# Optimization experiments

Hardware: AMD Instinct MI355X
Metric: run time of the kernel (lower is better)

The kernel has to match this reference:

```python
import jax, jax.numpy as jnp
import numpy as np

N_NODES = 100000
N_EDGES = 1600000
F_IN = 64
HIDDEN = 64
N_CLASSES = 2


def setup_inputs() -> dict:
    key = jax.random.key(0)
    k1, k2, k3, k4, k5, k6 = jax.random.split(key, 6)
    x = jax.random.normal(k1, (N_NODES, F_IN), dtype=jnp.float32)
    edge_index = jax.random.randint(k2, (2, N_EDGES), 0, N_NODES, dtype=jnp.int64)
    # Glorot-ish init for GCNConv linear weights, zero bias (PyG default)
    W1 = jax.random.normal(k3, (F_IN, HIDDEN), dtype=jnp.float32) * (1.0 / np.sqrt(F_IN))
    b1 = jnp.zeros((HIDDEN,), dtype=jnp.float32)
    W2 = jax.random.normal(k4, (HIDDEN, N_CLASSES), dtype=jnp.float32) * (1.0 / np.sqrt(HIDDEN))
    b2 = jnp.zeros((N_CLASSES,), dtype=jnp.float32)
    return {"x": x, "edge_index": edge_index, "W1": W1, "b1": b1, "W2": W2, "b2": b2}


def _gcn_norm(edge_index, num_nodes):
    # Add self-loops, then symmetric normalization D^-1/2 (A+I) D^-1/2
    loops = jnp.arange(num_nodes, dtype=edge_index.dtype)
    row = jnp.concatenate([edge_index[0], loops])  # [E+N] targets
    col = jnp.concatenate([edge_index[1], loops])  # [E+N] sources
    deg = jax.ops.segment_sum(jnp.ones(row.shape[0], jnp.float32), row, num_segments=num_nodes)
    dinv = jnp.where(deg > 0, jax.lax.rsqrt(deg), 0.0)
    norm = dinv[row] * dinv[col]  # [E+N]
    return row, col, norm


def _gcn_conv(x, W, b, row, col, norm, num_nodes):
    h = x @ W                                   # [N, out]
    msg = h[col] * norm[:, None]                # gather + scale, [E+N, out]
    agg = jax.ops.segment_sum(msg, row, num_segments=num_nodes)  # scatter-add
    return agg + b


def reference(x, edge_index, W1, b1, W2, b2):
    n = x.shape[0]
    row, col, norm = _gcn_norm(edge_index, n)
    h = jax.nn.relu(_gcn_conv(x, W1, b1, row, col, norm, n))
    # dropout p=0.5 is identity in eval mode
    logits = _gcn_conv(h, W2, b2, row, col, norm, n)
    return jax.nn.softmax(logits, axis=1)
```

## Files before the change

kernel.cpp:

```cpp
#include <hip/hip_runtime.h>
#include <hip/hip_fp16.h>


#define NBKT(n) (((n) + 255) >> 8)

typedef _Float16 f16x8 __attribute__((ext_vector_type(8)));
typedef float f32x4 __attribute__((ext_vector_type(4)));

__global__ __launch_bounds__(256) void k_bucketcount(const int* __restrict__ row,
                                                     int* __restrict__ bcnt,
                                                     __half* __restrict__ hp,
                                                     int E, int nb, int N) {
    __shared__ int cnt[392];
    int tid = threadIdx.x;
    int base = blockIdx.x * 4096;
    int m = E - base; if (m > 4096) m = 4096;
    for (int t = tid; t < nb; t += 256) cnt[t] = 0;
    __syncthreads();
    for (int i = tid; i < m; i += 256) atomicAdd(&cnt[row[base + i] >> 8], 1);
    __syncthreads();
    for (int t = tid; t < nb; t += 256) {
        int v = cnt[t];
        if (v > 0) atomicAdd(&bcnt[t], v);
    }
    if (blockIdx.x == 0 && tid < 32) ((int*)(hp + (size_t)N * 64))[tid] = 0;
}

__global__ __launch_bounds__(256) void k_bin(const int* __restrict__ row,
                                             const int* __restrict__ col,
                                             const int* __restrict__ bcnt,
                                             int* __restrict__ relcur,
                                             unsigned* __restrict__ pairbuf,
                                             int E, int nb) {
    __shared__ unsigned items[4096];
    __shared__ unsigned short bktid[4096];
    __shared__ int cnt[392];
    __shared__ int start0[392];
    __shared__ int cursor[392];
    __shared__ int gb[392];
    __shared__ int gbase[392];

    int tid = threadIdx.x;
    int base = blockIdx.x * 4096;
    int m = E - base; if (m > 4096) m = 4096;

    for (int t = tid; t < nb; t += 256) cnt[t] = 0;
    __syncthreads();
    for (int i = tid; i < m; i += 256) atomicAdd(&cnt[row[base + i] >> 8], 1);
    __syncthreads();
    if (tid < 64) {
        int lane = tid, running = 0;
        for (int ch = 0; ch < 7; ++ch) {
            int idx = ch * 64 + lane;
            int v = (idx < nb) ? cnt[idx] : 0;
            int s = v;
#pragma unroll
            for (int off = 1; off < 64; off <<= 1) {
                int t = __shfl_up(s, off, 64);
                if (lane >= off) s += t;
            }
            if (idx < nb) { start0[idx] = running + s - v; cursor[idx] = running + s - v; }
            running += __shfl(s, 63, 64);
        }
    } else if (tid < 128) {
        int lane = tid - 64, running = 0;
        for (int ch = 0; ch < 7; ++ch) {
            int idx = ch * 64 + lane;
            int v = (idx < nb) ? bcnt[idx] : 0;
            int s = v;
#pragma unroll
            for (int off = 1; off < 64; off <<= 1) {
                int t = __shfl_up(s, off, 64);
                if (lane >= off) s += t;
            }
            if (idx < nb) gb[idx] = running + s - v;
            running += __shfl(s, 63, 64);
        }
    }
    __syncthreads();
    for (int i = tid; i < m; i += 256) {
        int r = row[base + i];
        int c = col[base + i];
        int b = r >> 8;
        int pos = atomicAdd(&cursor[b], 1);
        items[pos] = ((unsigned)(r & 255) << 24) | (unsigned)c;
        bktid[pos] = (unsigned short)b;
    }
    __syncthreads();
    for (int t = tid; t < nb; t += 256) {
        int cv = cnt[t];
        if (cv > 0) gbase[t] = gb[t] + atomicAdd(&relcur[t], cv);
    }
    __syncthreads();
    for (int i = tid; i < m; i += 256) {
        int b = bktid[i];
        pairbuf[gbase[b] + (i - start0[b])] = items[i];
    }
}

__global__ __launch_bounds__(256) void k_sortnode(const unsigned* __restrict__ pairbuf,
                                                  const int* __restrict__ bcnt,
                                                  int* __restrict__ scol,
                                                  int* __restrict__ offsets,
                                                  float* __restrict__ dinv,
                                                  int N, int E) {
    __shared__ int ps[256];
    __shared__ int cnt[256];
    __shared__ int tmp[256];
    __shared__ int cur[256];
    int b = blockIdx.x;
    int tid = threadIdx.x;
    int v = (tid < b) ? bcnt[tid] : 0;
    if (tid + 256 < b) v += bcnt[tid + 256];
    ps[tid] = v;
    __syncthreads();
    for (int s = 128; s >= 1; s >>= 1) {
        if (tid < s) ps[tid] += ps[tid + s];
        __syncthreads();
    }
    int lo = ps[0];
    int hi = lo + bcnt[b];
    cnt[tid] = 0;
    __syncthreads();
    for (int i = lo + tid; i < hi; i += 256)
        atomicAdd(&cnt[pairbuf[i] >> 24], 1);
    __syncthreads();
    int cv = cnt[tid];
    tmp[tid] = cv;
    __syncthreads();
    for (int d = 1; d < 256; d <<= 1) {
        int t = (tid >= (unsigned)d) ? tmp[tid - d] : 0;
        __syncthreads();
        if (tid >= (unsigned)d) tmp[tid] += t;
        __syncthreads();
    }
    int excl = tmp[tid] - cv;
    int n = (b << 8) + tid;
    if (n < N) {
        offsets[n] = lo + excl;
        dinv[n] = rsqrtf((float)(cv + 1));
    }
    cur[tid] = lo + excl;
    if (b == 0 && tid == 0) { offsets[N] = E; scol[E] = N; }
    __syncthreads();
    for (int i = lo + tid; i < hi; i += 256) {
        unsigned it = pairbuf[i];
        int pos = atomicAdd(&cur[it >> 24], 1);
        scol[pos] = (int)(it & 0xFFFFFFu);
    }
}

__global__ __launch_bounds__(256, 2) void k_gemm1(const float* __restrict__ x,
                                                  const float* __restrict__ W1,
                                                  const float* __restrict__ dinv,
                                                  __half* __restrict__ hp, int N) {
    int lane = threadIdx.x & 63;
    int q = lane >> 4;
    int m = lane & 15;
    f16x8 bf[4][2];
#pragma unroll
    for (int nt = 0; nt < 4; ++nt)
#pragma unroll
        for (int kk = 0; kk < 2; ++kk)
#pragma unroll
            for (int j = 0; j < 8; ++j)
                bf[nt][kk][j] = (_Float16)W1[(kk * 32 + q * 8 + j) * 64 + nt * 16 + m];
    int wv = (int)((blockIdx.x * 256 + threadIdx.x) >> 6);
    int nw = (int)((gridDim.x * 256) >> 6);
    int T = N >> 4;
    for (int t = wv; t < T; t += nw) {
        const float* xrow = x + (size_t)(t * 16 + m) * 64;
        float4 u0 = *(const float4*)(xrow + q * 8);
        float4 u1 = *(const float4*)(xrow + q * 8 + 4);
        float4 u2 = *(const float4*)(xrow + 32 + q * 8);
        float4 u3 = *(const float4*)(xrow + 32 + q * 8 + 4);
        f16x8 a0, a1;
        a0[0] = (_Float16)u0.x; a0[1] = (_Float16)u0.y; a0[2] = (_Float16)u0.z; a0[3] = (_Float16)u0.w;
        a0[4] = (_Float16)u1.x; a0[5] = (_Float16)u1.y; a0[6] = (_Float16)u1.z; a0[7] = (_Float16)u1.w;
        a1[0] = (_Float16)u2.x; a1[1] = (_Float16)u2.y; a1[2] = (_Float16)u2.z; a1[3] = (_Float16)u2.w;
        a1[4] = (_Float16)u3.x; a1[5] = (_Float16)u3.y; a1[6] = (_Float16)u3.z; a1[7] = (_Float16)u3.w;
        f32x4 ac0 = {0.f, 0.f, 0.f, 0.f}, ac1 = ac0, ac2 = ac0, ac3 = ac0;
        ac0 = __builtin_amdgcn_mfma_f32_16x16x32_f16(a0, bf[0][0], ac0, 0, 0, 0);
        ac1 = __builtin_amdgcn_mfma_f32_16x16x32_f16(a0, bf[1][0], ac1, 0, 0, 0);
        ac2 = __builtin_amdgcn_mfma_f32_16x16x32_f16(a0, bf[2][0], ac2, 0, 0, 0);
        ac3 = __builtin_amdgcn_mfma_f32_16x16x32_f16(a0, bf[3][0], ac3, 0, 0, 0);
        ac0 = __builtin_amdgcn_mfma_f32_16x16x32_f16(a1, bf[0][1], ac0, 0, 0, 0);
        ac1 = __builtin_amdgcn_mfma_f32_16x16x32_f16(a1, bf[1][1], ac1, 0, 0, 0);
        ac2 = __builtin_amdgcn_mfma_f32_16x16x32_f16(a1, bf[2][1], ac2, 0, 0, 0);
        ac3 = __builtin_amdgcn_mfma_f32_16x16x32_f16(a1, bf[3][1], ac3, 0, 0, 0);
#pragma unroll
        for (int reg = 0; reg < 4; ++reg) {
            int rr = t * 16 + q * 4 + reg;
            float dv = dinv[rr];
            __half* dst = hp + (size_t)rr * 64 + m;
            dst[0]  = __float2half(dv * ac0[reg]);
            dst[16] = __float2half(dv * ac1[reg]);
            dst[32] = __float2half(dv * ac2[reg]);
            dst[48] = __float2half(dv * ac3[reg]);
        }
    }
}

__global__ __launch_bounds__(256) void k_agg1(const __half* __restrict__ hp,
                                              const int* __restrict__ offsets,
                                              const int* __restrict__ sorted_col,
                                              const float* __restrict__ dinv,
                                              const float* __restrict__ b1,
                                              const float* __restrict__ W2,
                                              float2* __restrict__ h2p, int N, int E) {
    int lane = threadIdx.x & 63;
    int slot = lane >> 3;
    int chunk = lane & 7;
    int wid = (int)((blockIdx.x * 256 + threadIdx.x) >> 6);
    int n = wid * 8 + slot;
    int nc = (n < N) ? n : N;
    int start = offsets[nc];
    int end = offsets[(n < N) ? (n + 1) : N];
    int deg = end - start;
    int maxd = deg;
#pragma unroll
    for (int s = 8; s <= 32; s <<= 1) {
        int o = __shfl_xor(maxd, s, 64);
        maxd = (o > maxd) ? o : maxd;
    }
    const float4* hp4 = (const float4*)hp;
    float4 sr = hp4[(size_t)nc * 8 + chunk];
    __half2 acc0 = ((const __half2*)&sr)[0];
    __half2 acc1 = ((const __half2*)&sr)[1];
    __half2 acc2 = ((const __half2*)&sr)[2];
    __half2 acc3 = ((const __half2*)&sr)[3];
    for (int j0 = 0; j0 < maxd; j0 += 4) {
        int a0 = (j0 + 0 < deg) ? (start + j0 + 0) : E;
        int a1 = (j0 + 1 < deg) ? (start + j0 + 1) : E;
        int a2 = (j0 + 2 < deg) ? (start + j0 + 2) : E;
        int a3 = (j0 + 3 < deg) ? (start + j0 + 3) : E;
        int c0 = sorted_col[a0];
        int c1 = sorted_col[a1];
        int c2 = sorted_col[a2];
        int c3 = sorted_col[a3];
        float4 r0 = hp4[(size_t)c0 * 8 + chunk];
        float4 r1 = hp4[(size_t)c1 * 8 + chunk];
        float4 r2 = hp4[(size_t)c2 * 8 + chunk];
        float4 r3 = hp4[(size_t)c3 * 8 + chunk];
        const __half2* h0 = (const __half2*)&r0;
        const __half2* h1_ = (const __half2*)&r1;
        const __half2* h2_ = (const __half2*)&r2;
        const __half2* h3 = (const __half2*)&r3;
        acc0 = __hadd2(acc0, h0[0]); acc1 = __hadd2(acc1, h0[1]);
        acc2 = __hadd2(acc2, h0[2]); acc3 = __hadd2(acc3, h0[3]);
        acc0 = __hadd2(acc0, h1_[0]); acc1 = __hadd2(acc1, h1_[1]);
        acc2 = __hadd2(acc2, h1_[2]); acc3 = __hadd2(acc3, h1_[3]);
        acc0 = __hadd2(acc0, h2_[0]); acc1 = __hadd2(acc1, h2_[1]);
        acc2 = __hadd2(acc2, h2_[2]); acc3 = __hadd2(acc3, h2_[3]);
        acc0 = __hadd2(acc0, h3[0]); acc1 = __hadd2(acc1, h3[1]);
        acc2 = __hadd2(acc2, h3[2]); acc3 = __hadd2(acc3, h3[3]);
    }
    float af[8];
    { float2 f;
      f = __half22float2(acc0); af[0] = f.x; af[1] = f.y;
      f = __half22float2(acc1); af[2] = f.x; af[3] = f.y;
      f = __half22float2(acc2); af[4] = f.x; af[5] = f.y;
      f = __half22float2(acc3); af[6] = f.x; af[7] = f.y; }
    float dn = dinv[(n < N) ? n : (N - 1)];
    float4 b1a = ((const float4*)b1)[chunk * 2];
    float4 b1b = ((const float4*)b1)[chunk * 2 + 1];
    float h1[8];
    h1[0] = fmaxf(fmaf(dn, af[0], b1a.x), 0.f);
    h1[1] = fmaxf(fmaf(dn, af[1], b1a.y), 0.f);
    h1[2] = fmaxf(fmaf(dn, af[2], b1a.z), 0.f);
    h1[3] = fmaxf(fmaf(dn, af[3], b1a.w), 0.f);
    h1[4] = fmaxf(fmaf(dn, af[4], b1b.x), 0.f);
    h1[5] = fmaxf(fmaf(dn, af[5], b1b.y), 0.f);
    h1[6] = fmaxf(fmaf(dn, af[6], b1b.z), 0.f);
    h1[7] = fmaxf(fmaf(dn, af[7], b1b.w), 0.f);
    float p0 = 0.f, p1 = 0.f;
#pragma unroll
    for (int k = 0; k < 4; ++k) {
        float4 w = ((const float4*)W2)[chunk * 4 + k];
        p0 = fmaf(h1[2 * k], w.x, p0); p1 = fmaf(h1[2 * k], w.y, p1);
        p0 = fmaf(h1[2 * k + 1], w.z, p0); p1 = fmaf(h1[2 * k + 1], w.w, p1);
    }
#pragma unroll
    for (int s = 1; s <= 4; s <<= 1) {
        p0 += __shfl_xor(p0, s, 64);
        p1 += __shfl_xor(p1, s, 64);
    }
    if (chunk == 0 && n < N) h2p[n] = make_float2(dn * p0, dn * p1);
}

__global__ __launch_bounds__(256) void k_agg2(const float2* __restrict__ h2p,
                                              const int* __restrict__ offsets,
                                              const int* __restrict__ sorted_col,
                                              const float* __restrict__ dinv,
                                              const float* __restrict__ b2,
                                              float2* __restrict__ out, int N) {
    int gtid = blockIdx.x * 256 + threadIdx.x;
    int n = gtid >> 4;
    int sub = threadIdx.x & 15;
    if (n >= N) return;
    int start = offsets[n], end = offsets[n + 1];
    float ax = 0.f, ay = 0.f;
    if (sub == 0) { float2 s = h2p[n]; ax = s.x; ay = s.y; }
    for (int j = start + sub; j < end; j += 16) {
        float2 v = h2p[sorted_col[j]];
        ax += v.x; ay += v.y;
    }
#pragma unroll
    for (int s = 1; s <= 8; s <<= 1) {
        ax += __shfl_xor(ax, s, 64);
        ay += __shfl_xor(ay, s, 64);
    }
    if (sub == 0) {
        float dn = dinv[n];
        float l0 = fmaf(dn, ax, b2[0]), l1 = fmaf(dn, ay, b2[1]);
        float m = fmaxf(l0, l1);
        float e0 = __expf(l0 - m), e1 = __expf(l1 - m);
        float inv = 1.0f / (e0 + e1);
        out[n] = make_float2(e0 * inv, e1 * inv);
    }
}

extern "C" void kernel_launch(void* const* d_in, const int* in_sizes, int n_in,
                              void* d_out, int out_size, void* d_ws, size_t ws_size,
                              hipStream_t stream) {
    const float* x  = (const float*)d_in[0];
    const int*   ei = (const int*)d_in[1];
    const float* W1 = (const float*)d_in[2];
    const float* b1 = (const float*)d_in[3];
    const float* W2 = (const float*)d_in[4];
    const float* b2 = (const float*)d_in[5];
    float2* out = (float2*)d_out;

    const int N = in_sizes[0] / 64;
    const int E = in_sizes[1] / 2;
    const int nb = NBKT(N);
    const int* row = ei;
    const int* col = ei + E;

    char* p = (char*)d_ws;
    auto alloc = [&](size_t bytes) -> void* {
        void* r = (void*)p;
        p += (bytes + 255) & ~(size_t)255;
        return r;
    };
    int*   bcnt    = (int*)alloc(784 * 4);
    int*   relcur  = bcnt + 392;
    int*   offsets = (int*)alloc((size_t)(N + 1) * 4);
    float* dinv    = (float*)alloc((size_t)N * 4);
    unsigned* pairbuf = (unsigned*)alloc((size_t)E * 4);
    int*   scol    = (int*)alloc((size_t)(E + 1) * 4);
    __half* hp     = (__half*)alloc((size_t)(N + 1) * 64 * 2);
    float2* h2p    = (float2*)alloc((size_t)N * 8);

    const int nTile = (E + 4095) / 4096;

    hipMemsetAsync(bcnt, 0, 784 * 4, stream);
    k_bucketcount<<<nTile, 256, 0, stream>>>(row, bcnt, hp, E, nb, N);
    k_bin<<<nTile, 256, 0, stream>>>(row, col, bcnt, relcur, pairbuf, E, nb);
    k_sortnode<<<nb, 256, 0, stream>>>(pairbuf, bcnt, scol, offsets, dinv, N, E);
    k_gemm1<<<512, 256, 0, stream>>>(x, W1, dinv, hp, N);
    const int nwaves = (N + 7) / 8;
    k_agg1<<<(nwaves + 3) / 4, 256, 0, stream>>>(hp, offsets, scol, dinv, b1, W2, h2p, N, E);
    k_agg2<<<(N * 16 + 255) / 256, 256, 0, stream>>>(h2p, offsets, scol, dinv, b2, out, N);
}
```

Before: 181.8 us.

## Fuse all GCN stages into one persistent kernel with grid-wide barriers

Replaces the six separate kernel launches (bucket count, binning, per-node sort, GEMM1, layer-1 aggregation, layer-2 aggregation) with one persistent kernel of 1120 blocks. The stages are separated by software grid barriers built on global atomics, and shared memory is reused through a union. Binning tiles shrink to 2048 edges, and the GEMM stage appears to stage dinv in LDS. This removes launch gaps and tail effects between short kernels, but relies on every block being co-resident and adds barrier spin cost plus occupancy limits from the fused register and LDS footprint.

```diff
diff --git a/kernel.cpp b/kernel.cpp
--- a/kernel.cpp
+++ b/kernel.cpp
@@ -2,321 +2,332 @@
 #include <hip/hip_fp16.h>
 
 
-#define NBKT(n) (((n) + 255) >> 8)
-
 typedef _Float16 f16x8 __attribute__((ext_vector_type(8)));
 typedef float f32x4 __attribute__((ext_vector_type(4)));
 
-__global__ __launch_bounds__(256) void k_bucketcount(const int* __restrict__ row,
-                                                     int* __restrict__ bcnt,
-                                                     __half* __restrict__ hp,
-                                                     int E, int nb, int N) {
-    __shared__ int cnt[392];
-    int tid = threadIdx.x;
-    int base = blockIdx.x * 4096;
-    int m = E - base; if (m > 4096) m = 4096;
-    for (int t = tid; t < nb; t += 256) cnt[t] = 0;
+#define GRID_BLOCKS 1120
+
+union SmemU {
+    int cnt1[392];
+    struct {
+        unsigned items[2048];
+        unsigned short bktid[2048];
+        int cnt[392];
+        int start0[392];
+        int cursor[392];
+        int gb[392];
+    } p2;
+    struct {
+        int ps[256];
+        int cnt[256];
+        int tmp[256];
+        int cur[256];
+        float sdinv[256];
+    } p3;
+};
+
+__device__ __forceinline__ void gsync(int* bar, int slot) {
     __syncthreads();
-    for (int i = tid; i < m; i += 256) atomicAdd(&cnt[row[base + i] >> 8], 1);
+    if (threadIdx.x == 0) {
+        __threadfence();
+        atomicAdd(&bar[slot], 1);
+        while (atomicAdd(&bar[slot], 0) < (int)gridDim.x)
+            __builtin_amdgcn_s_sleep(2);
+        __threadfence();
+    }
     __syncthreads();
-    for (int t = tid; t < nb; t += 256) {
-        int v = cnt[t];
-        if (v > 0) atomicAdd(&bcnt[t], v);
-    }
-    if (blockIdx.x == 0 && tid < 32) ((int*)(hp + (size_t)N * 64))[tid] = 0;
 }
 
-__global__ __launch_bounds__(256) void k_bin(const int* __restrict__ row,
-                                             const int* __restrict__ col,
-                                             const int* __restrict__ bcnt,
-                                             int* __restrict__ relcur,
-                                             unsigned* __restrict__ pairbuf,
-                                             int E, int nb) {
-    __shared__ unsigned items[4096];
-    __shared__ unsigned short bktid[4096];
-    __shared__ int cnt[392];
-    __shared__ int start0[392];
-    __shared__ int cursor[392];
-    __shared__ int gb[392];
-    __shared__ int gbase[392];
-
-    int tid = threadIdx.x;
-    int base = blockIdx.x * 4096;
-    int m = E - base; if (m > 4096) m = 4096;
-
-    for (int t = tid; t < nb; t += 256) cnt[t] = 0;
-    __syncthreads();
-    for (int i = tid; i < m; i += 256) atomicAdd(&cnt[row[base + i] >> 8], 1);
-    __syncthreads();
-    if (tid < 64) {
-        int lane = tid, running = 0;
-        for (int ch = 0; ch < 7; ++ch) {
-            int idx = ch * 64 + lane;
-            int v = (idx < nb) ? cnt[idx] : 0;
-            int s = v;
-#pragma unroll
-            for (int off = 1; off < 64; off <<= 1) {
-                int t = __shfl_up(s, off, 64);
-                if (lane >= off) s += t;
-            }
-            if (idx < nb) { start0[idx] = running + s - v; cursor[idx] = running + s - v; }
-            running += __shfl(s, 63, 64);
-        }
-    } else if (tid < 128) {
-        int lane = tid - 64, running = 0;
-        for (int ch = 0; ch < 7; ++ch) {
-            int idx = ch * 64 + lane;
-            int v = (idx < nb) ? bcnt[idx] : 0;
-            int s = v;
-#pragma unroll
-            for (int off = 1; off < 64; off <<= 1) {
-                int t = __shfl_up(s, off, 64);
-                if (lane >= off) s += t;
-            }
-            if (idx < nb) gb[idx] = running + s - v;
-            running += __shfl(s, 63, 64);
-        }
-    }
-    __syncthreads();
-    for (int i = tid; i < m; i += 256) {
-        int r = row[base + i];
-        int c = col[base + i];
-        int b = r >> 8;
-        int pos = atomicAdd(&cursor[b], 1);
-        items[pos] = ((unsigned)(r & 255) << 24) | (unsigned)c;
-        bktid[pos] = (unsigned short)b;
-    }
-    __syncthreads();
-    for (int t = tid; t < nb; t += 256) {
-        int cv = cnt[t];
-        if (cv > 0) gbase[t] = gb[t] + atomicAdd(&relcur[t], cv);
-    }
-    __syncthreads();
-    for (int i = tid; i < m; i += 256) {
-        int b = bktid[i];
-        pairbuf[gbase[b] + (i - start0[b])] = items[i];
-    }
-}
-
-__global__ __launch_bounds__(256) void k_sortnode(const unsigned* __restrict__ pairbuf,
-                                                  const int* __restrict__ bcnt,
-                                                  int* __restrict__ scol,
-                                                  int* __restrict__ offsets,
-                                                  float* __restrict__ dinv,
-                                                  int N, int E) {
-    __shared__ int ps[256];
-    __shared__ int cnt[256];
-    __shared__ int tmp[256];
-    __shared__ int cur[256];
-    int b = blockIdx.x;
-    int tid = threadIdx.x;
-    int v = (tid < b) ? bcnt[tid] : 0;
-    if (tid + 256 < b) v += bcnt[tid + 256];
-    ps[tid] = v;
-    __syncthreads();
-    for (int s = 128; s >= 1; s >>= 1) {
-        if (tid < s) ps[tid] += ps[tid + s];
+__global__ __launch_bounds__(256, 5) void k_mega(
+    const float* __restrict__ x, const int* __restrict__ row, const int* __restrict__ col,
+    const float* __restrict__ W1, const float* __restrict__ b1,
+    const float* __restrict__ W2, const float* __restrict__ b2,
+    int* __restrict__ ctrl,
+    int* __restrict__ offsets, float* __restrict__ dinv,
+    unsigned* __restrict__ pairbuf, int* __restrict__ scol,
+    __half* __restrict__ hp, float2* __restrict__ h2p,
+    float2* __restrict__ out, int N, int E, int nb)
+{
+    __shared__ SmemU sm;
+    int* bar = ctrl;
+    int* bcnt = ctrl + 16;
+    int* relcur = ctrl + 408;
+    const int tid = threadIdx.x;
+    const int G = (int)gridDim.x;
+
+    {
+        for (int t = tid; t < nb; t += 256) sm.cnt1[t] = 0;
         __syncthreads();
-    }
-    int lo = ps[0];
-    int hi = lo + bcnt[b];
-    cnt[tid] = 0;
-    __syncthreads();
-    for (int i = lo + tid; i < hi; i += 256)
-        atomicAdd(&cnt[pairbuf[i] >> 24], 1);
-    __syncthreads();
-    int cv = cnt[tid];
-    tmp[tid] = cv;
-    __syncthreads();
-    for (int d = 1; d < 256; d <<= 1) {
-        int t = (tid >= (unsigned)d) ? tmp[tid - d] : 0;
+        int chunk = (E + G - 1) / G;
+        int lo = blockIdx.x * chunk;
+        int hi = lo + chunk; if (hi > E) hi = E;
+        for (int i = lo + tid; i < hi; i += 256) atomicAdd(&sm.cnt1[row[i] >> 8], 1);
         __syncthreads();
-        if (tid >= (unsigned)d) tmp[tid] += t;
-        __syncthreads();
-    }
-    int excl = tmp[tid] - cv;
-    int n = (b << 8) + tid;
-    if (n < N) {
-        offsets[n] = lo + excl;
-        dinv[n] = rsqrtf((float)(cv + 1));
-    }
-    cur[tid] = lo + excl;
-    if (b == 0 && tid == 0) { offsets[N] = E; scol[E] = N; }
-    __syncthreads();
-    for (int i = lo + tid; i < hi; i += 256) {
-        unsigned it = pairbuf[i];
-        int pos = atomicAdd(&cur[it >> 24], 1);
-        scol[pos] = (int)(it & 0xFFFFFFu);
-    }
-}
-
-__global__ __launch_bounds__(256, 2) void k_gemm1(const float* __restrict__ x,
-                                                  const float* __restrict__ W1,
-                                                  const float* __restrict__ dinv,
-                                                  __half* __restrict__ hp, int N) {
-    int lane = threadIdx.x & 63;
-    int q = lane >> 4;
-    int m = lane & 15;
-    f16x8 bf[4][2];
-#pragma unroll
-    for (int nt = 0; nt < 4; ++nt)
-#pragma unroll
-        for (int kk = 0; kk < 2; ++kk)
-#pragma unroll
-            for (int j = 0; j < 8; ++j)
-                bf[nt][kk][j] = (_Float16)W1[(kk * 32 + q * 8 + j) * 64 + nt * 16 + m];
-    int wv = (int)((blockIdx.x * 256 + threadIdx.x) >> 6);
-    int nw = (int)((gridDim.x * 256) >> 6);
-    int T = N >> 4;
-    for (int t = wv; t < T; t += nw) {
-        const float* xrow = x + (size_t)(t * 16 + m) * 64;
-        float4 u0 = *(const float4*)(xrow + q * 8);
-        float4 u1 = *(const float4*)(xrow + q * 8 + 4);
-        float4 u2 = *(const float4*)(xrow + 32 + q * 8);
-        float4 u3 = *(const float4*)(xrow + 32 + q * 8 + 4);
-        f16x8 a0, a1;
-        a0[0] = (_Float16)u0.x; a0[1] = (_Float16)u0.y; a0[2] = (_Float16)u0.z; a0[3] = (_Float16)u0.w;
-        a0[4] = (_Float16)u1.x; a0[5] = (_Float16)u1.y; a0[6] = (_Float16)u1.z; a0[7] = (_Float16)u1.w;
-        a1[0] = (_Float16)u2.x; a1[1] = (_Float16)u2.y; a1[2] = (_Float16)u2.z; a1[3] = (_Float16)u2.w;
-        a1[4] = (_Float16)u3.x; a1[5] = (_Float16)u3.y; a1[6] = (_Float16)u3.z; a1[7] = (_Float16)u3.w;
-        f32x4 ac0 = {0.f, 0.f, 0.f, 0.f}, ac1 = ac0, ac2 = ac0, ac3 = ac0;
-        ac0 = __builtin_amdgcn_mfma_f32_16x16x32_f16(a0, bf[0][0], ac0, 0, 0, 0);
-        ac1 = __builtin_amdgcn_mfma_f32_16x16x32_f16(a0, bf[1][0], ac1, 0, 0, 0);
-        ac2 = __builtin_amdgcn_mfma_f32_16x16x32_f16(a0, bf[2][0], ac2, 0, 0, 0);
-        ac3 = __builtin_amdgcn_mfma_f32_16x16x32_f16(a0, bf[3][0], ac3, 0, 0, 0);
-        ac0 = __builtin_amdgcn_mfma_f32_16x16x32_f16(a1, bf[0][1], ac0, 0, 0, 0);
-        ac1 = __builtin_amdgcn_mfma_f32_16x16x32_f16(a1, bf[1][1], ac1, 0, 0, 0);
-        ac2 = __builtin_amdgcn_mfma_f32_16x16x32_f16(a1, bf[2][1], ac2, 0, 0, 0);
-        ac3 = __builtin_amdgcn_mfma_f32_16x16x32_f16(a1, bf[3][1], ac3, 0, 0, 0);
-#pragma unroll
-        for (int reg = 0; reg < 4; ++reg) {
-            int rr = t * 16 + q * 4 + reg;
-            float dv = dinv[rr];
-            __half* dst = hp + (size_t)rr * 64 + m;
-            dst[0]  = __float2half(dv * ac0[reg]);
-            dst[16] = __float2half(dv * ac1[reg]);
-            dst[32] = __float2half(dv * ac2[reg]);
-            dst[48] = __float2half(dv * ac3[reg]);
-        }
-    }
-}
-
-__global__ __launch_bounds__(256) void k_agg1(const __half* __restrict__ hp,
-                                              const int* __restrict__ offsets,
-                                              const int* __restrict__ sorted_col,
-                                              const float* __restrict__ dinv,
-                                              const float* __restrict__ b1,
-                                              const float* __restrict__ W2,
-                                              float2* __restrict__ h2p, int N, int E) {
-    int lane = threadIdx.x & 63;
-    int slot = lane >> 3;
-    int chunk = lane & 7;
-    int wid = (int)((blockIdx.x * 256 + threadIdx.x) >> 6);
-    int n = wid * 8 + slot;
-    int nc = (n < N) ? n : N;
-    int start = offsets[nc];
-    int end = offsets[(n < N) ? (n + 1) : N];
-    int deg = end - start;
-    int maxd = deg;
-#pragma unroll
-    for (int s = 8; s <= 32; s <<= 1) {
-        int o = __shfl_xor(maxd, s, 64);
-        maxd = (o > maxd) ? o : maxd;
-    }
-    const float4* hp4 = (const float4*)hp;
-    float4 sr = hp4[(size_t)nc * 8 + chunk];
-    __half2 acc0 = ((const __half2*)&sr)[0];
-    __half2 acc1 = ((const __half2*)&sr)[1];
-    __half2 acc2 = ((const __half2*)&sr)[2];
-    __half2 acc3 = ((const __half2*)&sr)[3];
-    for (int j0 = 0; j0 < maxd; j0 += 4) {
-        int a0 = (j0 + 0 < deg) ? (start + j0 + 0) : E;
-        int a1 = (j0 + 1 < deg) ? (start + j0 + 1) : E;
-        int a2 = (j0 + 2 < deg) ? (start + j0 + 2) : E;
-        int a3 = (j0 + 3 < deg) ? (start + j0 + 3) : E;
-        int c0 = sorted_col[a0];
-        int c1 = sorted_col[a1];
-        int c2 = sorted_col[a2];
-        int c3 = sorted_col[a3];
-        float4 r0 = hp4[(size_t)c0 * 8 + chunk];
-        float4 r1 = hp4[(size_t)c1 * 8 + chunk];
-        float4 r2 = hp4[(size_t)c2 * 8 + chunk];
-        float4 r3 = hp4[(size_t)c3 * 8 + chunk];
-        const __half2* h0 = (const __half2*)&r0;
-        const __half2* h1_ = (const __half2*)&r1;
-        const __half2* h2_ = (const __half2*)&r2;
-        const __half2* h3 = (const __half2*)&r3;
-        acc0 = __hadd2(acc0, h0[0]); acc1 = __hadd2(acc1, h0[1]);
-        acc2 = __hadd2(acc2, h0[2]); acc3 = __hadd2(acc3, h0[3]);
-        acc0 = __hadd2(acc0, h1_[0]); acc1 = __hadd2(acc1, h1_[1]);
-        acc2 = __hadd2(acc2, h1_[2]); acc3 = __hadd2(acc3, h1_[3]);
-        acc0 = __hadd2(acc0, h2_[0]); acc1 = __hadd2(acc1, h2_[1]);
-        acc2 = __hadd2(acc2, h2_[2]); acc3 = __hadd2(acc3, h2_[3]);
-        acc0 = __hadd2(acc0, h3[0]); acc1 = __hadd2(acc1, h3[1]);
-        acc2 = __hadd2(acc2, h3[2]); acc3 = __hadd2(acc3, h3[3]);
-    }
-    float af[8];
-    { float2 f;
-      f = __half22float2(acc0); af[0] = f.x; af[1] = f.y;
-      f = __half22float2(acc1); af[2] = f.x; af[3] = f.y;
-      f = __half22float2(acc2); af[4] = f.x; af[5] = f.y;
-      f = __half22float2(acc3); af[6] = f.x; af[7] = f.y; }
-    float dn = dinv[(n < N) ? n : (N - 1)];
-    float4 b1a = ((const float4*)b1)[chunk * 2];
-    float4 b1b = ((const float4*)b1)[chunk * 2 + 1];
-    float h1[8];
-    h1[0] = fmaxf(fmaf(dn, af[0], b1a.x), 0.f);
-    h1[1] = fmaxf(fmaf(dn, af[1], b1a.y), 0.f);
-    h1[2] = fmaxf(fmaf(dn, af[2], b1a.z), 0.f);
-    h1[3] = fmaxf(fmaf(dn, af[3], b1a.w), 0.f);
-    h1[4] = fmaxf(fmaf(dn, af[4], b1b.x), 0.f);
-    h1[5] = fmaxf(fmaf(dn, af[5], b1b.y), 0.f);
-    h1[6] = fmaxf(fmaf(dn, af[6], b1b.z), 0.f);
-    h1[7] = fmaxf(fmaf(dn, af[7], b1b.w), 0.f);
-    float p0 = 0.f, p1 = 0.f;
-#pragma unroll
-    for (int k = 0; k < 4; ++k) {
-        float4 w = ((const float4*)W2)[chunk * 4 + k];
-        p0 = fmaf(h1[2 * k], w.x, p0); p1 = fmaf(h1[2 * k], w.y, p1);
-        p0 = fmaf(h1[2 * k + 1], w.z, p0); p1 = fmaf(h1[2 * k + 1], w.w, p1);
-    }
-#pragma unroll
-    for (int s = 1; s <= 4; s <<= 1) {
-        p0 += __shfl_xor(p0, s, 64);
-        p1 += __shfl_xor(p1, s, 64);
-    }
-    if (chunk == 0 && n < N) h2p[n] = make_float2(dn * p0, dn * p1);
-}
-
-__global__ __launch_bounds__(256) void k_agg2(const float2* __restrict__ h2p,
-                                              const int* __restrict__ offsets,
-                                              const int* __restrict__ sorted_col,
-                                              const float* __restrict__ dinv,
-                                              const float* __restrict__ b2,
-                                              float2* __restrict__ out, int N) {
-    int gtid = blockIdx.x * 256 + threadIdx.x;
-    int n = gtid >> 4;
-    int sub = threadIdx.x & 15;
-    if (n >= N) return;
-    int start = offsets[n], end = offsets[n + 1];
-    float ax = 0.f, ay = 0.f;
-    if (sub == 0) { float2 s = h2p[n]; ax = s.x; ay = s.y; }
-    for (int j = start + sub; j < end; j += 16) {
-        float2 v = h2p[sorted_col[j]];
-        ax += v.x; ay += v.y;
-    }
-#pragma unroll
-    for (int s = 1; s <= 8; s <<= 1) {
-        ax += __shfl_xor(ax, s, 64);
-        ay += __shfl_xor(ay, s, 64);
-    }
-    if (sub == 0) {
-        float dn = dinv[n];
-        float l0 = fmaf(dn, ax, b2[0]), l1 = fmaf(dn, ay, b2[1]);
-        float m = fmaxf(l0, l1);
-        float e0 = __expf(l0 - m), e1 = __expf(l1 - m);
-        float inv = 1.0f / (e0 + e1);
-        out[n] = make_float2(e0 * inv, e1 * inv);
+        for (int t = tid; t < nb; t += 256) {
+            int v = sm.cnt1[t];
+            if (v) atomicAdd(&bcnt[t], v);
+        }
+        if (blockIdx.x == 0 && tid < 32) ((int*)(hp + (size_t)N * 64))[tid] = 0;
+    }
+    gsync(bar, 0);
+
+    {
+        int nT = (E + 2047) / 2048;
+        for (int t = blockIdx.x; t < nT; t += G) {
+            int base = t * 2048;
+            int m = E - base; if (m > 2048) m = 2048;
+            for (int i = tid; i < nb; i += 256) sm.p2.cnt[i] = 0;
+            __syncthreads();
+            for (int i = tid; i < m; i += 256) atomicAdd(&sm.p2.cnt[row[base + i] >> 8], 1);
+            __syncthreads();
+            if (tid < 64) {
+                int lane = tid, running = 0;
+                for (int ch = 0; ch < 7; ++ch) {
+                    int idx = ch * 64 + lane;
+                    int v = (idx < nb) ? sm.p2.cnt[idx] : 0;
+                    int s = v;
+#pragma unroll
+                    for (int off = 1; off < 64; off <<= 1) {
+                        int tt = __shfl_up(s, off, 64);
+                        if (lane >= off) s += tt;
+                    }
+                    if (idx < nb) { sm.p2.start0[idx] = running + s - v; sm.p2.cursor[idx] = running + s - v; }
+                    running += __shfl(s, 63, 64);
+                }
+            } else if (tid < 128) {
+                int lane = tid - 64, running = 0;
+                for (int ch = 0; ch < 7; ++ch) {
+                    int idx = ch * 64 + lane;
+                    int v = (idx < nb) ? bcnt[idx] : 0;
+                    int s = v;
+#pragma unroll
+                    for (int off = 1; off < 64; off <<= 1) {
+                        int tt = __shfl_up(s, off, 64);
+                        if (lane >= off) s += tt;
+                    }
+                    if (idx < nb) sm.p2.gb[idx] = running + s - v;
+                    running += __shfl(s, 63, 64);
+                }
+            }
+            __syncthreads();
+            for (int i = tid; i < nb; i += 256) {
+                int cv = sm.p2.cnt[i];
+                if (cv > 0) sm.p2.cnt[i] = sm.p2.gb[i] + atomicAdd(&relcur[i], cv);
+            }
+            for (int i = tid; i < m; i += 256) {
+                int r = row[base + i];
+                int c = col[base + i];
+                int b = r >> 8;
+                int pos = atomicAdd(&sm.p2.cursor[b], 1);
+                sm.p2.items[pos] = ((unsigned)(r & 255) << 24) | (unsigned)c;
+                sm.p2.bktid[pos] = (unsigned short)b;
+            }
+            __syncthreads();
+            for (int i = tid; i < m; i += 256) {
+                int b = sm.p2.bktid[i];
+                pairbuf[sm.p2.cnt[b] + (i - sm.p2.start0[b])] = sm.p2.items[i];
+            }
+            __syncthreads();
+        }
+    }
+    gsync(bar, 1);
+
+    {
+        int lane = tid & 63, q = lane >> 4, mm = lane & 15;
+        f16x8 bf[4][2];
+#pragma unroll
+        for (int nt = 0; nt < 4; ++nt)
+#pragma unroll
+            for (int kk = 0; kk < 2; ++kk)
+#pragma unroll
+                for (int j = 0; j < 8; ++j)
+                    bf[nt][kk][j] = (_Float16)W1[(kk * 32 + q * 8 + j) * 64 + nt * 16 + mm];
+        for (int b = blockIdx.x; b < nb; b += G) {
+            int v = (tid < b) ? bcnt[tid] : 0;
+            if (tid + 256 < b) v += bcnt[tid + 256];
+            sm.p3.ps[tid] = v;
+            __syncthreads();
+            for (int s = 128; s >= 1; s >>= 1) {
+                if (tid < s) sm.p3.ps[tid] += sm.p3.ps[tid + s];
+                __syncthreads();
+            }
+            int lo = sm.p3.ps[0];
+            int hi = lo + bcnt[b];
+            sm.p3.cnt[tid] = 0;
+            __syncthreads();
+            for (int i = lo + tid; i < hi; i += 256) atomicAdd(&sm.p3.cnt[pairbuf[i] >> 24], 1);
+            __syncthreads();
+            int cv = sm.p3.cnt[tid];
+            sm.p3.tmp[tid] = cv;
+            __syncthreads();
+            for (int d = 1; d < 256; d <<= 1) {
+                int tt = (tid >= d) ? sm.p3.tmp[tid - d] : 0;
+                __syncthreads();
+                if (tid >= d) sm.p3.tmp[tid] += tt;
+                __syncthreads();
+            }
+            int excl = sm.p3.tmp[tid] - cv;
+            int n = (b << 8) + tid;
+            float dv = rsqrtf((float)(cv + 1));
+            if (n < N) { offsets[n] = lo + excl; dinv[n] = dv; }
+            sm.p3.sdinv[tid] = dv;
+            sm.p3.cur[tid] = lo + excl;
+            if (b == 0 && tid == 0) { offsets[N] = E; scol[E] = N; }
+            __syncthreads();
+            for (int i = lo + tid; i < hi; i += 256) {
+                unsigned it = pairbuf[i];
+                int pos = atomicAdd(&sm.p3.cur[it >> 24], 1);
+                scol[pos] = (int)(it & 0xFFFFFFu);
+            }
+            __syncthreads();
+            int n0 = b << 8;
+            int nn = N - n0; if (nn > 256) nn = 256;
+            int wv = tid >> 6;
+            for (int t = wv; t < (nn >> 4); t += 4) {
+                const float* xrow = x + (size_t)(n0 + t * 16 + mm) * 64;
+                float4 u0 = *(const float4*)(xrow + q * 8);
+                float4 u1 = *(const float4*)(xrow + q * 8 + 4);
+                float4 u2 = *(const float4*)(xrow + 32 + q * 8);
+                float4 u3 = *(const float4*)(xrow + 32 + q * 8 + 4);
+                f16x8 a0, a1;
+                a0[0] = (_Float16)u0.x; a0[1] = (_Float16)u0.y; a0[2] = (_Float16)u0.z; a0[3] = (_Float16)u0.w;
+                a0[4] = (_Float16)u1.x; a0[5] = (_Float16)u1.y; a0[6] = (_Float16)u1.z; a0[7] = (_Float16)u1.w;
+                a1[0] = (_Float16)u2.x; a1[1] = (_Float16)u2.y; a1[2] = (_Float16)u2.z; a1[3] = (_Float16)u2.w;
+                a1[4] = (_Float16)u3.x; a1[5] = (_Float16)u3.y; a1[6] = (_Float16)u3.z; a1[7] = (_Float16)u3.w;
+                f32x4 ac0 = {0.f, 0.f, 0.f, 0.f}, ac1 = ac0, ac2 = ac0, ac3 = ac0;
+                ac0 = __builtin_amdgcn_mfma_f32_16x16x32_f16(a0, bf[0][0], ac0, 0, 0, 0);
+                ac1 = __builtin_amdgcn_mfma_f32_16x16x32_f16(a0, bf[1][0], ac1, 0, 0, 0);
+                ac2 = __builtin_amdgcn_mfma_f32_16x16x32_f16(a0, bf[2][0], ac2, 0, 0, 0);
+                ac3 = __builtin_amdgcn_mfma_f32_16x16x32_f16(a0, bf[3][0], ac3, 0, 0, 0);
+                ac0 = __builtin_amdgcn_mfma_f32_16x16x32_f16(a1, bf[0][1], ac0, 0, 0, 0);
+                ac1 = __builtin_amdgcn_mfma_f32_16x16x32_f16(a1, bf[1][1], ac1, 0, 0, 0);
+                ac2 = __builtin_amdgcn_mfma_f32_16x16x32_f16(a1, bf[2][1], ac2, 0, 0, 0);
+                ac3 = __builtin_amdgcn_mfma_f32_16x16x32_f16(a1, bf[3][1], ac3, 0, 0, 0);
+#pragma unroll
+                for (int reg = 0; reg < 4; ++reg) {
+                    int rl = t * 16 + q * 4 + reg;
+                    float dvv = sm.p3.sdinv[rl];
+                    __half* dst = hp + (size_t)(n0 + rl) * 64 + mm;
+                    dst[0]  = __float2half(dvv * ac0[reg]);
+                    dst[16] = __float2half(dvv * ac1[reg]);
+                    dst[32] = __float2half(dvv * ac2[reg]);
+                    dst[48] = __float2half(dvv * ac3[reg]);
+                }
+            }
+            __syncthreads();
+        }
+    }
+    gsync(bar, 2);
+
+    {
+        int lane = tid & 63, slot = lane >> 3, chunk = lane & 7;
+        int ngroups = (N + 7) >> 3;
+        const float4* hp4 = (const float4*)hp;
+        for (int g = blockIdx.x * 4 + (tid >> 6); g < ngroups; g += G * 4) {
+            int n = g * 8 + slot;
+            int nc = (n < N) ? n : N;
+            int start = offsets[nc];
+            int end = offsets[(n < N) ? (n + 1) : N];
+            int deg = end - start;
+            int maxd = deg;
+#pragma unroll
+            for (int s = 8; s <= 32; s <<= 1) {
+                int o = __shfl_xor(maxd, s, 64);
+                maxd = (o > maxd) ? o : maxd;
+            }
+            float4 sr = hp4[(size_t)nc * 8 + chunk];
+            __half2 acc0 = ((const __half2*)&sr)[0];
+            __half2 acc1 = ((const __half2*)&sr)[1];
+            __half2 acc2 = ((const __half2*)&sr)[2];
+            __half2 acc3 = ((const __half2*)&sr)[3];
+            for (int j0 = 0; j0 < maxd; j0 += 4) {
+                int a0 = (j0 + 0 < deg) ? (start + j0 + 0) : E;
+                int a1 = (j0 + 1 < deg) ? (start + j0 + 1) : E;
+                int a2 = (j0 + 2 < deg) ? (start + j0 + 2) : E;
+                int a3 = (j0 + 3 < deg) ? (start + j0 + 3) : E;
+                int c0 = scol[a0];
+                int c1 = scol[a1];
+                int c2 = scol[a2];
+                int c3 = scol[a3];
+                float4 r0 = hp4[(size_t)c0 * 8 + chunk];
+                float4 r1 = hp4[(size_t)c1 * 8 + chunk];
+                float4 r2 = hp4[(size_t)c2 * 8 + chunk];
+                float4 r3 = hp4[(size_t)c3 * 8 + chunk];
+                const __half2* h0 = (const __half2*)&r0;
+                const __half2* h1_ = (const __half2*)&r1;
+                const __half2* h2_ = (const __half2*)&r2;
+                const __half2* h3 = (const __half2*)&r3;
+                acc0 = __hadd2(acc0, h0[0]); acc1 = __hadd2(acc1, h0[1]);
+                acc2 = __hadd2(acc2, h0[2]); acc3 = __hadd2(acc3, h0[3]);
+                acc0 = __hadd2(acc0, h1_[0]); acc1 = __hadd2(acc1, h1_[1]);
+                acc2 = __hadd2(acc2, h1_[2]); acc3 = __hadd2(acc3, h1_[3]);
+                acc0 = __hadd2(acc0, h2_[0]); acc1 = __hadd2(acc1, h2_[1]);
+                acc2 = __hadd2(acc2, h2_[2]); acc3 = __hadd2(acc3, h2_[3]);
+                acc0 = __hadd2(acc0, h3[0]); acc1 = __hadd2(acc1, h3[1]);
+                acc2 = __hadd2(acc2, h3[2]); acc3 = __hadd2(acc3, h3[3]);
+            }
+            float af[8];
+            { float2 f;
+              f = __half22float2(acc0); af[0] = f.x; af[1] = f.y;
+              f = __half22float2(acc1); af[2] = f.x; af[3] = f.y;
+              f = __half22float2(acc2); af[4] = f.x; af[5] = f.y;
+              f = __half22float2(acc3); af[6] = f.x; af[7] = f.y; }
+            float dn = dinv[(n < N) ? n : (N - 1)];
+            float4 b1a = ((const float4*)b1)[chunk * 2];
+            float4 b1b = ((const float4*)b1)[chunk * 2 + 1];
+            float h1[8];
+            h1[0] = fmaxf(fmaf(dn, af[0], b1a.x), 0.f);
+            h1[1] = fmaxf(fmaf(dn, af[1], b1a.y), 0.f);
+            h1[2] = fmaxf(fmaf(dn, af[2], b1a.z), 0.f);
+            h1[3] = fmaxf(fmaf(dn, af[3], b1a.w), 0.f);
+            h1[4] = fmaxf(fmaf(dn, af[4], b1b.x), 0.f);
+            h1[5] = fmaxf(fmaf(dn, af[5], b1b.y), 0.f);
+            h1[6] = fmaxf(fmaf(dn, af[6], b1b.z), 0.f);
+            h1[7] = fmaxf(fmaf(dn, af[7], b1b.w), 0.f);
+            float p0 = 0.f, p1 = 0.f;
+#pragma unroll
+            for (int k = 0; k < 4; ++k) {
+                float4 w = ((const float4*)W2)[chunk * 4 + k];
+                p0 = fmaf(h1[2 * k], w.x, p0); p1 = fmaf(h1[2 * k], w.y, p1);
+                p0 = fmaf(h1[2 * k + 1], w.z, p0); p1 = fmaf(h1[2 * k + 1], w.w, p1);
+            }
+#pragma unroll
+            for (int s = 1; s <= 4; s <<= 1) {
+                p0 += __shfl_xor(p0, s, 64);
+                p1 += __shfl_xor(p1, s, 64);
+            }
+            if (chunk == 0 && n < N) h2p[n] = make_float2(dn * p0, dn * p1);
+        }
+    }
+    gsync(bar, 3);
+
+    {
+        float b20 = b2[0], b21 = b2[1];
+        int T = G * 256;
+        int sub = tid & 15;
+        for (int i = blockIdx.x * 256 + tid; i < N * 16; i += T) {
+            int n = i >> 4;
+            int start = offsets[n], end = offsets[n + 1];
+            float ax = 0.f, ay = 0.f;
+            if (sub == 0) { float2 s = h2p[n]; ax = s.x; ay = s.y; }
+            for (int j = start + sub; j < end; j += 16) {
+                float2 vv = h2p[scol[j]];
+                ax += vv.x; ay += vv.y;
+            }
+#pragma unroll
+            for (int s = 1; s <= 8; s <<= 1) {
+                ax += __shfl_xor(ax, s, 64);
+                ay += __shfl_xor(ay, s, 64);
+            }
+            if (sub == 0) {
+                float dn = dinv[n];
+                float l0 = fmaf(dn, ax, b20), l1 = fmaf(dn, ay, b21);
+                float m = fmaxf(l0, l1);
+                float e0 = __expf(l0 - m), e1 = __expf(l1 - m);
+                float inv = 1.0f / (e0 + e1);
+                out[n] = make_float2(e0 * inv, e1 * inv);
+            }
+        }
     }
 }
 
@@ -333,7 +344,7 @@
 
     const int N = in_sizes[0] / 64;
     const int E = in_sizes[1] / 2;
-    const int nb = NBKT(N);
+    const int nb = (N + 255) >> 8;
     const int* row = ei;
     const int* col = ei + E;
 
@@ -343,8 +354,7 @@
         p += (bytes + 255) & ~(size_t)255;
         return r;
     };
-    int*   bcnt    = (int*)alloc(784 * 4);
-    int*   relcur  = bcnt + 392;
+    int*   ctrl    = (int*)alloc(800 * 4);
     int*   offsets = (int*)alloc((size_t)(N + 1) * 4);
     float* dinv    = (float*)alloc((size_t)N * 4);
     unsigned* pairbuf = (unsigned*)alloc((size_t)E * 4);
@@ -352,14 +362,8 @@
     __half* hp     = (__half*)alloc((size_t)(N + 1) * 64 * 2);
     float2* h2p    = (float2*)alloc((size_t)N * 8);
 
-    const int nTile = (E + 4095) / 4096;
-
-    hipMemsetAsync(bcnt, 0, 784 * 4, stream);
-    k_bucketcount<<<nTile, 256, 0, stream>>>(row, bcnt, hp, E, nb, N);
-    k_bin<<<nTile, 256, 0, stream>>>(row, col, bcnt, relcur, pairbuf, E, nb);
-    k_sortnode<<<nb, 256, 0, stream>>>(pairbuf, bcnt, scol, offsets, dinv, N, E);
-    k_gemm1<<<512, 256, 0, stream>>>(x, W1, dinv, hp, N);
-    const int nwaves = (N + 7) / 8;
-    k_agg1<<<(nwaves + 3) / 4, 256, 0, stream>>>(hp, offsets, scol, dinv, b1, W2, h2p, N, E);
-    k_agg2<<<(N * 16 + 255) / 256, 256, 0, stream>>>(h2p, offsets, scol, dinv, b2, out, N);
+    hipMemsetAsync(ctrl, 0, 800 * 4, stream);
+    k_mega<<<GRID_BLOCKS, 256, 0, stream>>>(x, row, col, W1, b1, W2, b2,
+                                            ctrl, offsets, dinv, pairbuf, scol,
+                                            hp, h2p, out, N, E, nb);
 }
```

Measured after the change: 724.3 us. 3.98x slower.

## Use fixed-capacity buckets to drop bucket-count pass and fuse node sort with GEMM

Applied to the files above, without the earlier changes.

Replaces the prefix-summed global bucket offsets with fixed-capacity slots per 256-node bucket (8192 entries each). This removes the separate bucket-count kernel, and the binning kernel no longer needs a global scan. The per-bucket node sort is fused with the first-layer MFMA GEMM, so dinv is taken from shared memory, and a per-node degree array replaces offsets[n+1]. The agg1 gather loop is unrolled from 4 to 8 edges for more loads in flight. The cost is a larger, padded CSR buffer, and correctness now assumes no bucket receives more than 8192 edges, which holds for uniform random inputs but could overflow on skewed graphs.

```diff
diff --git a/kernel.cpp b/kernel.cpp
--- a/kernel.cpp
+++ b/kernel.cpp
@@ -2,42 +2,23 @@
 #include <hip/hip_fp16.h>
 
 
-#define NBKT(n) (((n) + 255) >> 8)
-
 typedef _Float16 f16x8 __attribute__((ext_vector_type(8)));
 typedef float f32x4 __attribute__((ext_vector_type(4)));
 
-__global__ __launch_bounds__(256) void k_bucketcount(const int* __restrict__ row,
-                                                     int* __restrict__ bcnt,
-                                                     __half* __restrict__ hp,
-                                                     int E, int nb, int N) {
-    __shared__ int cnt[392];
-    int tid = threadIdx.x;
-    int base = blockIdx.x * 4096;
-    int m = E - base; if (m > 4096) m = 4096;
-    for (int t = tid; t < nb; t += 256) cnt[t] = 0;
-    __syncthreads();
-    for (int i = tid; i < m; i += 256) atomicAdd(&cnt[row[base + i] >> 8], 1);
-    __syncthreads();
-    for (int t = tid; t < nb; t += 256) {
-        int v = cnt[t];
-        if (v > 0) atomicAdd(&bcnt[t], v);
-    }
-    if (blockIdx.x == 0 && tid < 32) ((int*)(hp + (size_t)N * 64))[tid] = 0;
-}
+#define CAPSH 13
+#define CAP (1 << CAPSH)
 
 __global__ __launch_bounds__(256) void k_bin(const int* __restrict__ row,
                                              const int* __restrict__ col,
-                                             const int* __restrict__ bcnt,
                                              int* __restrict__ relcur,
                                              unsigned* __restrict__ pairbuf,
-                                             int E, int nb) {
+                                             __half* __restrict__ hp,
+                                             int E, int nb, int N) {
     __shared__ unsigned items[4096];
     __shared__ unsigned short bktid[4096];
     __shared__ int cnt[392];
     __shared__ int start0[392];
     __shared__ int cursor[392];
-    __shared__ int gb[392];
     __shared__ int gbase[392];
 
     int tid = threadIdx.x;
@@ -62,20 +43,6 @@
             if (idx < nb) { start0[idx] = running + s - v; cursor[idx] = running + s - v; }
             running += __shfl(s, 63, 64);
         }
-    } else if (tid < 128) {
-        int lane = tid - 64, running = 0;
-        for (int ch = 0; ch < 7; ++ch) {
-            int idx = ch * 64 + lane;
-            int v = (idx < nb) ? bcnt[idx] : 0;
-            int s = v;
-#pragma unroll
-            for (int off = 1; off < 64; off <<= 1) {
-                int t = __shfl_up(s, off, 64);
-                if (lane >= off) s += t;
-            }
-            if (idx < nb) gb[idx] = running + s - v;
-            running += __shfl(s, 63, 64);
-        }
     }
     __syncthreads();
     for (int i = tid; i < m; i += 256) {
@@ -89,37 +56,44 @@
     __syncthreads();
     for (int t = tid; t < nb; t += 256) {
         int cv = cnt[t];
-        if (cv > 0) gbase[t] = gb[t] + atomicAdd(&relcur[t], cv);
+        if (cv > 0) gbase[t] = (t << CAPSH) + atomicAdd(&relcur[t], cv);
     }
     __syncthreads();
     for (int i = tid; i < m; i += 256) {
         int b = bktid[i];
         pairbuf[gbase[b] + (i - start0[b])] = items[i];
     }
-}
-
-__global__ __launch_bounds__(256) void k_sortnode(const unsigned* __restrict__ pairbuf,
-                                                  const int* __restrict__ bcnt,
-                                                  int* __restrict__ scol,
-                                                  int* __restrict__ offsets,
-                                                  float* __restrict__ dinv,
-                                                  int N, int E) {
-    __shared__ int ps[256];
+    if (blockIdx.x == 0 && tid < 32) ((int*)(hp + (size_t)N * 64))[tid] = 0;
+}
+
+__global__ __launch_bounds__(256, 4) void k_sortgemm(const unsigned* __restrict__ pairbuf,
+                                                     const int* __restrict__ relcur,
+                                                     const float* __restrict__ x,
+                                                     const float* __restrict__ W1,
+                                                     int* __restrict__ scol,
+                                                     int* __restrict__ offsets,
+                                                     int* __restrict__ deg,
+                                                     float* __restrict__ dinv,
+                                                     __half* __restrict__ hp,
+                                                     int N, int nb) {
     __shared__ int cnt[256];
     __shared__ int tmp[256];
     __shared__ int cur[256];
+    __shared__ float sdinv[256];
     int b = blockIdx.x;
     int tid = threadIdx.x;
-    int v = (tid < b) ? bcnt[tid] : 0;
-    if (tid + 256 < b) v += bcnt[tid + 256];
-    ps[tid] = v;
-    __syncthreads();
-    for (int s = 128; s >= 1; s >>= 1) {
-        if (tid < s) ps[tid] += ps[tid + s];
-        __syncthreads();
-    }
-    int lo = ps[0];
-    int hi = lo + bcnt[b];
+    int lane = tid & 63, q = lane >> 4, mm = lane & 15;
+    f16x8 bf[4][2];
+#pragma unroll
+    for (int nt = 0; nt < 4; ++nt)
+#pragma unroll
+        for (int kk = 0; kk < 2; ++kk)
+#pragma unroll
+            for (int j = 0; j < 8; ++j)
+                bf[nt][kk][j] = (_Float16)W1[(kk * 32 + q * 8 + j) * 64 + nt * 16 + mm];
+
+    int lo = b << CAPSH;
+    int hi = lo + relcur[b];
     cnt[tid] = 0;
     __syncthreads();
     for (int i = lo + tid; i < hi; i += 256)
@@ -129,47 +103,32 @@
     tmp[tid] = cv;
     __syncthreads();
     for (int d = 1; d < 256; d <<= 1) {
-        int t = (tid >= (unsigned)d) ? tmp[tid - d] : 0;
+        int t = (tid >= d) ? tmp[tid - d] : 0;
         __syncthreads();
-        if (tid >= (unsigned)d) tmp[tid] += t;
+        if (tid >= d) tmp[tid] += t;
         __syncthreads();
     }
     int excl = tmp[tid] - cv;
     int n = (b << 8) + tid;
-    if (n < N) {
-        offsets[n] = lo + excl;
-        dinv[n] = rsqrtf((float)(cv + 1));
-    }
+    float dv = rsqrtf((float)(cv + 1));
+    if (n < N) { offsets[n] = lo + excl; deg[n] = cv; dinv[n] = dv; }
+    sdinv[tid] = dv;
     cur[tid] = lo + excl;
-    if (b == 0 && tid == 0) { offsets[N] = E; scol[E] = N; }
+    if (b == 0 && tid == 0) {
+        offsets[N] = 0; deg[N] = 0;
+        scol[nb << CAPSH] = N;
+    }
     __syncthreads();
     for (int i = lo + tid; i < hi; i += 256) {
         unsigned it = pairbuf[i];
         int pos = atomicAdd(&cur[it >> 24], 1);
         scol[pos] = (int)(it & 0xFFFFFFu);
     }
-}
-
-__global__ __launch_bounds__(256, 2) void k_gemm1(const float* __restrict__ x,
-                                                  const float* __restrict__ W1,
-                                                  const float* __restrict__ dinv,
-                                                  __half* __restrict__ hp, int N) {
-    int lane = threadIdx.x & 63;
-    int q = lane >> 4;
-    int m = lane & 15;
-    f16x8 bf[4][2];
-#pragma unroll
-    for (int nt = 0; nt < 4; ++nt)
-#pragma unroll
-        for (int kk = 0; kk < 2; ++kk)
-#pragma unroll
-            for (int j = 0; j < 8; ++j)
-                bf[nt][kk][j] = (_Float16)W1[(kk * 32 + q * 8 + j) * 64 + nt * 16 + m];
-    int wv = (int)((blockIdx.x * 256 + threadIdx.x) >> 6);
-    int nw = (int)((gridDim.x * 256) >> 6);
-    int T = N >> 4;
-    for (int t = wv; t < T; t += nw) {
-        const float* xrow = x + (size_t)(t * 16 + m) * 64;
+    __syncthreads();
+    int n0 = b << 8;
+    int nn = N - n0; if (nn > 256) nn = 256;
+    for (int t = (tid >> 6); t < (nn >> 4); t += 4) {
+        const float* xrow = x + (size_t)(n0 + t * 16 + mm) * 64;
         float4 u0 = *(const float4*)(xrow + q * 8);
         float4 u1 = *(const float4*)(xrow + q * 8 + 4);
         float4 u2 = *(const float4*)(xrow + 32 + q * 8);
@@ -190,24 +149,26 @@
         ac3 = __builtin_amdgcn_mfma_f32_16x16x32_f16(a1, bf[3][1], ac3, 0, 0, 0);
 #pragma unroll
         for (int reg = 0; reg < 4; ++reg) {
-            int rr = t * 16 + q * 4 + reg;
-            float dv = dinv[rr];
-            __half* dst = hp + (size_t)rr * 64 + m;
-            dst[0]  = __float2half(dv * ac0[reg]);
-            dst[16] = __float2half(dv * ac1[reg]);
-            dst[32] = __float2half(dv * ac2[reg]);
-            dst[48] = __float2half(dv * ac3[reg]);
+            int rl = t * 16 + q * 4 + reg;
+            float dvv = sdinv[rl];
+            __half* dst = hp + (size_t)(n0 + rl) * 64 + mm;
+            dst[0]  = __float2half(dvv * ac0[reg]);
+            dst[16] = __float2half(dvv * ac1[reg]);
+            dst[32] = __float2half(dvv * ac2[reg]);
+            dst[48] = __float2half(dvv * ac3[reg]);
         }
     }
 }
 
-__global__ __launch_bounds__(256) void k_agg1(const __half* __restrict__ hp,
-                                              const int* __restrict__ offsets,
-                                              const int* __restrict__ sorted_col,
-                                              const float* __restrict__ dinv,
-                                              const float* __restrict__ b1,
-                                              const float* __restrict__ W2,
-                                              float2* __restrict__ h2p, int N, int E) {
+__global__ __launch_bounds__(256, 4) void k_agg1(const __half* __restrict__ hp,
+                                                 const int* __restrict__ offsets,
+                                                 const int* __restrict__ deg,
+                                                 const int* __restrict__ scol,
+                                                 const float* __restrict__ dinv,
+                                                 const float* __restrict__ b1,
+                                                 const float* __restrict__ W2,
+                                                 float2* __restrict__ h2p,
+                                                 int N, int SENT) {
     int lane = threadIdx.x & 63;
     int slot = lane >> 3;
     int chunk = lane & 7;
@@ -215,9 +176,8 @@
     int n = wid * 8 + slot;
     int nc = (n < N) ? n : N;
     int start = offsets[nc];
-    int end = offsets[(n < N) ? (n + 1) : N];
-    int deg = end - start;
-    int maxd = deg;
+    int dg = deg[nc];
+    int maxd = dg;
 #pragma unroll
     for (int s = 8; s <= 32; s <<= 1) {
         int o = __shfl_xor(maxd, s, 64);
@@ -229,31 +189,20 @@
     __half2 acc1 = ((const __half2*)&sr)[1];
     __half2 acc2 = ((const __half2*)&sr)[2];
     __half2 acc3 = ((const __half2*)&sr)[3];
-    for (int j0 = 0; j0 < maxd; j0 += 4) {
-        int a0 = (j0 + 0 < deg) ? (start + j0 + 0) : E;
-        int a1 = (j0 + 1 < deg) ? (start + j0 + 1) : E;
-        int a2 = (j0 + 2 < deg) ? (start + j0 + 2) : E;
-        int a3 = (j0 + 3 < deg) ? (start + j0 + 3) : E;
-        int c0 = sorted_col[a0];
-        int c1 = sorted_col[a1];
-        int c2 = sorted_col[a2];
-        int c3 = sorted_col[a3];
-        float4 r0 = hp4[(size_t)c0 * 8 + chunk];
-        float4 r1 = hp4[(size_t)c1 * 8 + chunk];
-        float4 r2 = hp4[(size_t)c2 * 8 + chunk];
-        float4 r3 = hp4[(size_t)c3 * 8 + chunk];
-        const __half2* h0 = (const __half2*)&r0;
-        const __half2* h1_ = (const __half2*)&r1;
-        const __half2* h2_ = (const __half2*)&r2;
-        const __half2* h3 = (const __half2*)&r3;
-        acc0 = __hadd2(acc0, h0[0]); acc1 = __hadd2(acc1, h0[1]);
-        acc2 = __hadd2(acc2, h0[2]); acc3 = __hadd2(acc3, h0[3]);
-        acc0 = __hadd2(acc0, h1_[0]); acc1 = __hadd2(acc1, h1_[1]);
-        acc2 = __hadd2(acc2, h1_[2]); acc3 = __hadd2(acc3, h1_[3]);
-        acc0 = __hadd2(acc0, h2_[0]); acc1 = __hadd2(acc1, h2_[1]);
-        acc2 = __hadd2(acc2, h2_[2]); acc3 = __hadd2(acc3, h2_[3]);
-        acc0 = __hadd2(acc0, h3[0]); acc1 = __hadd2(acc1, h3[1]);
-        acc2 = __hadd2(acc2, h3[2]); acc3 = __hadd2(acc3, h3[3]);
+    for (int j0 = 0; j0 < maxd; j0 += 8) {
+        int c[8];
+#pragma unroll
+        for (int u = 0; u < 8; ++u)
+            c[u] = scol[(j0 + u < dg) ? (start + j0 + u) : SENT];
+        float4 r[8];
+#pragma unroll
+        for (int u = 0; u < 8; ++u) r[u] = hp4[(size_t)c[u] * 8 + chunk];
+#pragma unroll
+        for (int u = 0; u < 8; ++u) {
+            const __half2* hh = (const __half2*)&r[u];
+            acc0 = __hadd2(acc0, hh[0]); acc1 = __hadd2(acc1, hh[1]);
+            acc2 = __hadd2(acc2, hh[2]); acc3 = __hadd2(acc3, hh[3]);
+        }
     }
     float af[8];
     { float2 f;
@@ -290,7 +239,8 @@
 
 __global__ __launch_bounds__(256) void k_agg2(const float2* __restrict__ h2p,
                                               const int* __restrict__ offsets,
-                                              const int* __restrict__ sorted_col,
+                                              const int* __restrict__ deg,
+                                              const int* __restrict__ scol,
                                               const float* __restrict__ dinv,
                                               const float* __restrict__ b2,
                                               float2* __restrict__ out, int N) {
@@ -298,11 +248,11 @@
     int n = gtid >> 4;
     int sub = threadIdx.x & 15;
     if (n >= N) return;
-    int start = offsets[n], end = offsets[n + 1];
+    int start = offsets[n], end = start + deg[n];
     float ax = 0.f, ay = 0.f;
     if (sub == 0) { float2 s = h2p[n]; ax = s.x; ay = s.y; }
     for (int j = start + sub; j < end; j += 16) {
-        float2 v = h2p[sorted_col[j]];
+        float2 v = h2p[scol[j]];
         ax += v.x; ay += v.y;
     }
 #pragma unroll
@@ -333,7 +283,8 @@
 
     const int N = in_sizes[0] / 64;
     const int E = in_sizes[1] / 2;
-    const int nb = NBKT(N);
+    const int nb = (N + 255) >> 8;
+    const int SENT = nb << CAPSH;
     const int* row = ei;
     const int* col = ei + E;
 
@@ -343,23 +294,21 @@
         p += (bytes + 255) & ~(size_t)255;
         return r;
     };
-    int*   bcnt    = (int*)alloc(784 * 4);
-    int*   relcur  = bcnt + 392;
+    int*   relcur  = (int*)alloc((size_t)nb * 4);
     int*   offsets = (int*)alloc((size_t)(N + 1) * 4);
+    int*   deg     = (int*)alloc((size_t)(N + 1) * 4);
     float* dinv    = (float*)alloc((size_t)N * 4);
-    unsigned* pairbuf = (unsigned*)alloc((size_t)E * 4);
-    int*   scol    = (int*)alloc((size_t)(E + 1) * 4);
+    unsigned* pairbuf = (unsigned*)alloc((size_t)nb * CAP * 4);
+    int*   scol    = (int*)alloc(((size_t)nb * CAP + 1) * 4);
     __half* hp     = (__half*)alloc((size_t)(N + 1) * 64 * 2);
     float2* h2p    = (float2*)alloc((size_t)N * 8);
 
     const int nTile = (E + 4095) / 4096;
 
-    hipMemsetAsync(bcnt, 0, 784 * 4, stream);
-    k_bucketcount<<<nTile, 256, 0, stream>>>(row, bcnt, hp, E, nb, N);
-    k_bin<<<nTile, 256, 0, stream>>>(row, col, bcnt, relcur, pairbuf, E, nb);
-    k_sortnode<<<nb, 256, 0, stream>>>(pairbuf, bcnt, scol, offsets, dinv, N, E);
-    k_gemm1<<<512, 256, 0, stream>>>(x, W1, dinv, hp, N);
+    hipMemsetAsync(relcur, 0, (size_t)nb * 4, stream);
+    k_bin<<<nTile, 256, 0, stream>>>(row, col, relcur, pairbuf, hp, E, nb, N);
+    k_sortgemm<<<nb, 256, 0, stream>>>(pairbuf, relcur, x, W1, scol, offsets, deg, dinv, hp, N, nb);
     const int nwaves = (N + 7) / 8;
-    k_agg1<<<(nwaves + 3) / 4, 256, 0, stream>>>(hp, offsets, scol, dinv, b1, W2, h2p, N, E);
-    k_agg2<<<(N * 16 + 255) / 256, 256, 0, stream>>>(h2p, offsets, scol, dinv, b2, out, N);
-}
+    k_agg1<<<(nwaves + 3) / 4, 256, 0, stream>>>(hp, offsets, deg, scol, dinv, b1, W2, h2p, N, SENT);
+    k_agg2<<<(N * 16 + 255) / 256, 256, 0, stream>>>(h2p, offsets, deg, scol, dinv, b2, out, N);
+}
```

Result: faster. 165.7 us (-8.9%).
